# Performance work log

Hardware: AMD Instinct MI355X
Metric: run time of the kernel (lower is better)

The kernel has to match this reference:

```python
import jax, jax.numpy as jnp
import numpy as np

N = 50000      # nodes
E = 800000     # edges
DIM = 64       # dim_h (= input_dim)
H = 4          # heads
D = DIM // H   # per-head dim = 16
EDGE_DIM = 16
L = 5          # conv layers
G = 64         # graphs in batch
FINAL = 1
SCALE = 1.0 / np.sqrt(D)


def setup_inputs() -> dict:
    key = jax.random.key(0)
    ks = jax.random.split(key, 12)
    x = jax.random.normal(ks[0], (N, DIM), jnp.float32)
    edge_index = jax.random.randint(ks[1], (2, E), 0, N, dtype=jnp.int32).astype(jnp.int64)
    edge_attr = jax.random.normal(ks[2], (E, EDGE_DIM), jnp.float32)
    batch = jnp.sort(jax.random.randint(ks[3], (N,), 0, G, dtype=jnp.int32).astype(jnp.int64))
    s = 1.0 / np.sqrt(DIM)
    se = 1.0 / np.sqrt(EDGE_DIM)
    Wq = jax.random.normal(ks[4], (L, DIM, DIM), jnp.float32) * s
    Wk = jax.random.normal(ks[5], (L, DIM, DIM), jnp.float32) * s
    Wv = jax.random.normal(ks[6], (L, DIM, DIM), jnp.float32) * s
    We = jax.random.normal(ks[7], (L, EDGE_DIM, DIM), jnp.float32) * se
    Wskip = jax.random.normal(ks[8], (L, DIM, DIM), jnp.float32) * s
    W1 = jax.random.normal(ks[9], (L * DIM, L * DIM), jnp.float32) * (1.0 / np.sqrt(L * DIM))
    b1 = jnp.zeros((L * DIM,), jnp.float32)
    W2 = jax.random.normal(ks[10], (L * DIM, FINAL), jnp.float32) * (1.0 / np.sqrt(L * DIM))
    b2 = jnp.zeros((FINAL,), jnp.float32)
    return dict(x=x, edge_index=edge_index, edge_attr=edge_attr, batch=batch,
                Wq=Wq, Wk=Wk, Wv=Wv, We=We, Wskip=Wskip, W1=W1, b1=b1, W2=W2, b2=b2)


def _conv(x, Wq, Wk, Wv, We, Wsk, src, dst, edge_attr):
    # Edge-featured multi-head attention conv (EINv1 / TransformerConv-style).
    n = x.shape[0]
    q = (x @ Wq).reshape(n, H, D)[dst]                      # [E,H,D] query from dst node
    e = (edge_attr @ We).reshape(-1, H, D)                  # [E,H,D] edge projection
    k = (x @ Wk).reshape(n, H, D)[src] + e                  # [E,H,D]
    v = (x @ Wv).reshape(n, H, D)[src] + e                  # [E,H,D]
    logits = (q * k).sum(-1) * SCALE                        # [E,H]
    m = jax.ops.segment_max(logits, dst, num_segments=n)    # per-dst-node max
    a = jnp.exp(logits - m[dst])
    s = jax.ops.segment_sum(a, dst, num_segments=n)
    alpha = a / (s[dst] + 1e-16)                            # segment softmax over incoming edges
    agg = jax.ops.segment_sum(alpha[..., None] * v, dst, num_segments=n)  # [N,H,D]
    return agg.reshape(n, H * D) + x @ Wsk                  # root/skip connection


def reference(x, edge_index, edge_attr, batch, Wq, Wk, Wv, We, Wskip, W1, b1, W2, b2):
    src, dst = edge_index[0], edge_index[1]
    counts = jax.ops.segment_sum(jnp.ones((x.shape[0],), x.dtype), batch, num_segments=G)
    denom = jnp.maximum(counts, 1.0)[:, None]
    h = x
    pooled = []
    for l in range(L):  # fixed small layer count
        h = jax.nn.relu(_conv(h, Wq[l], Wk[l], Wv[l], We[l], Wskip[l], src, dst, edge_attr))
        pooled.append(jax.ops.segment_sum(h, batch, num_segments=G) / denom)  # global_mean_pool
    hcat = jnp.concatenate(pooled, axis=1)                  # [G, 5*DIM]
    hid = jax.nn.relu(hcat @ W1 + b1)
    out = hid @ W2 + b2                                     # dropout is identity in eval
    return out.reshape(-1)                                  # flatten -> [G*FINAL]
```

## Files before the change

kernel.cpp:

```cpp
#include <hip/hip_runtime.h>
#include <math.h>

#define NN 50000
#define NE 800000
#define GG 64
#define SCAN_BLK 512
#define SCAN_NB ((NN + SCAN_BLK - 1) / SCAN_BLK)
#define CSR_CAP (NE + 4 * NN)
#define NBLK ((NN + 63) / 64)

typedef unsigned int uint;
typedef unsigned short ushort;
typedef __attribute__((ext_vector_type(8))) short short8v;
typedef __attribute__((ext_vector_type(4))) float f32x4;

__device__ __forceinline__ uint bf16r(float x) {
    uint u = __float_as_uint(x);
    return (u + 0x7fffu + ((u >> 16) & 1u)) >> 16;
}

__device__ __forceinline__ float red8(float x) {
    float t;
    t = __int_as_float(__builtin_amdgcn_update_dpp(0, __float_as_int(x), 0xB1, 0xF, 0xF, 1));
    x += t;
    t = __int_as_float(__builtin_amdgcn_update_dpp(0, __float_as_int(x), 0x4E, 0xF, 0xF, 1));
    x += t;
    t = __int_as_float(__builtin_amdgcn_update_dpp(0, __float_as_int(x), 0x141, 0xF, 0xF, 1));
    x += t;
    return x;
}


__global__ __launch_bounds__(256) void k_degrank(const int* __restrict__ dstv,
                                                 int* __restrict__ deg,
                                                 int* __restrict__ rank) {
    int e = blockIdx.x * 256 + threadIdx.x;
    if (e < NE) rank[e] = atomicAdd(&deg[dstv[e]], 1);
}

__global__ __launch_bounds__(SCAN_BLK) void k_scan1(const int* __restrict__ deg,
                                                    int* __restrict__ locoff,
                                                    int* __restrict__ bsum) {
    __shared__ int sh[SCAN_BLK];
    int tid = threadIdx.x;
    int n = blockIdx.x * SCAN_BLK + tid;
    int v = (n < NN) ? ((deg[n] + 3) & ~3) : 0;
    sh[tid] = v;
    __syncthreads();
    for (int off = 1; off < SCAN_BLK; off <<= 1) {
        int t = (tid >= off) ? sh[tid - off] : 0;
        __syncthreads();
        sh[tid] += t;
        __syncthreads();
    }
    if (n < NN) locoff[n] = sh[tid] - v;
    if (tid == SCAN_BLK - 1) bsum[blockIdx.x] = sh[tid];
}

__global__ void k_scan2b(int* __restrict__ bsum,
                         const int* __restrict__ batch,
                         int* __restrict__ bstart,
                         float* __restrict__ inv,
                         int* __restrict__ ntot) {
    __shared__ int sh[128];
    __shared__ int sb[65];
    int t = threadIdx.x;
    int v = (t < SCAN_NB) ? bsum[t] : 0;
    sh[t] = v;
    __syncthreads();
    for (int off = 1; off < 128; off <<= 1) {
        int u = (t >= off) ? sh[t - off] : 0;
        __syncthreads();
        sh[t] += u;
        __syncthreads();
    }
    if (t < SCAN_NB) bsum[t] = sh[t] - v;
    if (t == 127) ntot[0] = sh[127];
    if (t <= 64) {
        int lo = 0, hi = NN;
        while (lo < hi) { int mid = (lo + hi) >> 1; if (batch[mid] < t) lo = mid + 1; else hi = mid; }
        sb[t] = lo;
        bstart[t] = lo;
    }
    __syncthreads();
    if (t < 64) inv[t] = 1.0f / fmaxf((float)(sb[t + 1] - sb[t]), 1.0f);
}

__global__ __launch_bounds__(256) void k_scatter(const int* __restrict__ srcv,
                                                 const int* __restrict__ dstv,
                                                 const int* __restrict__ locoff,
                                                 const int* __restrict__ bsum,
                                                 const int* __restrict__ rank,
                                                 const int* __restrict__ deg,
                                                 int* __restrict__ srcp,
                                                 int* __restrict__ e2p) {
    int idx = blockIdx.x * 256 + threadIdx.x;
    if (idx < NE) {
        int d = dstv[idx];
        int p = locoff[d] + bsum[d >> 9] + rank[idx];
        srcp[p] = srcv[idx] << 8;
        e2p[p] = idx;
    } else if (idx < NE + NN) {
        int nd = idx - NE;
        int start = locoff[nd] + bsum[nd >> 9];
        int dgn = deg[nd];
        int al = (dgn + 3) & ~3;
        for (int p = start + dgn; p < start + al; ++p) {
            srcp[p] = 0;
            e2p[p] = 0;
        }
    }
}

__global__ __launch_bounds__(256) void k_gather(const int* __restrict__ e2p,
                                                const float* __restrict__ eattr,
                                                uint* __restrict__ aperm32,
                                                const int* __restrict__ ntot) {
    int tot = ntot[0];
    for (int p = blockIdx.x * 256 + threadIdx.x; p < tot; p += gridDim.x * 256) {
        int e = e2p[p];
        const float4* ea = reinterpret_cast<const float4*>(eattr + (size_t)e * 16);
        float4 a = ea[0], b = ea[1], c = ea[2], d4 = ea[3];
        uint u0 = bf16r(a.x) | (bf16r(a.y) << 16);
        uint u1 = bf16r(a.z) | (bf16r(a.w) << 16);
        uint u2 = bf16r(b.x) | (bf16r(b.y) << 16);
        uint u3 = bf16r(b.z) | (bf16r(b.w) << 16);
        uint u4 = bf16r(c.x) | (bf16r(c.y) << 16);
        uint u5 = bf16r(c.z) | (bf16r(c.w) << 16);
        uint u6 = bf16r(d4.x) | (bf16r(d4.y) << 16);
        uint u7 = bf16r(d4.z) | (bf16r(d4.w) << 16);
        uint* base = aperm32 + (size_t)(p >> 2) * 32 + (p & 1) * 16 + ((p >> 1) & 1);
        base[0]  = u0;  base[2]  = u1;  base[4]  = u2;  base[6]  = u3;
        base[8]  = u4;  base[10] = u5;  base[12] = u6;  base[14] = u7;
    }
}


__global__ __launch_bounds__(256) void k_wfrag(const float* __restrict__ Wq,
                                               const float* __restrict__ Wk,
                                               const float* __restrict__ Wv,
                                               const float* __restrict__ Wsk,
                                               const float* __restrict__ We,
                                               ushort* __restrict__ Wf) {
    int t = blockIdx.x * 256 + threadIdx.x;
    if (t >= 5 * 20 * 2 * 64) return;
    int l = t / (20 * 2 * 64);
    int rem = t % (20 * 2 * 64);
    int nt = rem >> 7, s = (rem >> 6) & 1, lane = rem & 63;
    int c = nt * 16 + (lane & 15);
    int k0 = s * 32 + 8 * (lane >> 4);
    int msel = c >> 6, cc = c & 63;
    const float C2 = 0.36067376022224085f;
    ushort o[8];
    if (msel == 4) {
        int hh = cc >> 4, ja = cc & 15;
        const float* we = We + l * 1024 + ja * 64 + hh * 16;
#pragma unroll
        for (int j = 0; j < 8; ++j) {
            const float* wq = Wq + l * 4096 + (k0 + j) * 64 + hh * 16;
            float acc = 0.f;
#pragma unroll
            for (int dd = 0; dd < 16; ++dd) acc += wq[dd] * we[dd];
            o[j] = (ushort)bf16r(acc * C2);
        }
    } else {
        const float* W = (msel == 0) ? Wq + l * 4096 :
                         (msel == 1) ? Wk + l * 4096 :
                         (msel == 2) ? Wv + l * 4096 : Wsk + l * 4096;
        float sc = (msel == 0) ? C2 : 1.0f;
#pragma unroll
        for (int j = 0; j < 8; ++j) o[j] = (ushort)bf16r(W[(k0 + j) * 64 + cc] * sc);
    }
    uint4* dst = reinterpret_cast<uint4*>(Wf + (size_t)t * 8);
    uint4 u;
    u.x = (uint)o[0] | ((uint)o[1] << 16);
    u.y = (uint)o[2] | ((uint)o[3] << 16);
    u.z = (uint)o[4] | ((uint)o[5] << 16);
    u.w = (uint)o[6] | ((uint)o[7] << 16);
    dst[0] = u;
}


template<bool L0>
__global__ __launch_bounds__(256) void k_projm(const float* __restrict__ x,
                                               const ushort* __restrict__ Hin,
                                               const ushort* __restrict__ Wfl,
                                               uint* __restrict__ QQp,
                                               uint* __restrict__ KVp,
                                               ushort* __restrict__ Sbh) {
    int tid = threadIdx.x, lane = tid & 63, wv = tid >> 6;
    int n0 = blockIdx.x * 64;
    int arow = lane & 15, agrp = lane >> 4;

    short8v A[4][2];
#pragma unroll
    for (int mt = 0; mt < 4; ++mt) {
        int node = n0 + mt * 16 + arow;
        if (node >= NN) node = NN - 1;
#pragma unroll
        for (int s = 0; s < 2; ++s) {
            int k0 = s * 32 + agrp * 8;
            if (L0) {
                const float* hp = x + (size_t)node * 64 + k0;
                float4 u = *reinterpret_cast<const float4*>(hp);
                float4 v = *reinterpret_cast<const float4*>(hp + 4);
                short8v a;
                a[0] = (short)bf16r(u.x); a[1] = (short)bf16r(u.y);
                a[2] = (short)bf16r(u.z); a[3] = (short)bf16r(u.w);
                a[4] = (short)bf16r(v.x); a[5] = (short)bf16r(v.y);
                a[6] = (short)bf16r(v.z); a[7] = (short)bf16r(v.w);
                A[mt][s] = a;
            } else {
                A[mt][s] = *reinterpret_cast<const short8v*>(Hin + (size_t)node * 64 + k0);
            }
        }
    }

    int ch = wv * 16 + arow;
    int rb = agrp * 4;
    f32x4 qh[4], kh[4];
    const f32x4 z = {0.f, 0.f, 0.f, 0.f};

#pragma unroll
    for (int ni = 0; ni < 5; ++ni) {
        int ntl = wv + 4 * ni;
        f32x4 acc[4] = {z, z, z, z};
#pragma unroll
        for (int s = 0; s < 2; ++s) {
            short8v B = *reinterpret_cast<const short8v*>(
                Wfl + (((size_t)ntl * 2 + s) * 64 + lane) * 8);
#pragma unroll
            for (int mt = 0; mt < 4; ++mt)
                acc[mt] = __builtin_amdgcn_mfma_f32_16x16x32_bf16(A[mt][s], B, acc[mt], 0, 0, 0);
        }
        if (ni == 0) {
#pragma unroll
            for (int mt = 0; mt < 4; ++mt) qh[mt] = acc[mt];
        } else if (ni == 1) {
#pragma unroll
            for (int mt = 0; mt < 4; ++mt) kh[mt] = acc[mt];
        } else if (ni == 2) {
#pragma unroll
            for (int mt = 0; mt < 4; ++mt)
#pragma unroll
                for (int r = 0; r < 4; ++r) {
                    int node = n0 + mt * 16 + rb + r;
                    if (node < NN)
                        KVp[(size_t)node * 64 + ch] = (bf16r(kh[mt][r]) << 16) | bf16r(acc[mt][r]);
                }
        } else if (ni == 3) {
#pragma unroll
            for (int mt = 0; mt < 4; ++mt)
#pragma unroll
                for (int r = 0; r < 4; ++r) {
                    int node = n0 + mt * 16 + rb + r;
                    if (node < NN) Sbh[(size_t)node * 64 + ch] = (ushort)bf16r(acc[mt][r]);
                }
        } else {
#pragma unroll
            for (int mt = 0; mt < 4; ++mt)
#pragma unroll
                for (int r = 0; r < 4; ++r) {
                    int node = n0 + mt * 16 + rb + r;
                    if (node < NN)
                        QQp[(size_t)node * 64 + ch] = (bf16r(qh[mt][r]) << 16) | bf16r(acc[mt][r]);
                }
        }
    }
}


__global__ __launch_bounds__(256) void k_attn(const uint* __restrict__ QQp,
                                              const uint* __restrict__ KVp,
                                              const ushort* __restrict__ Sbh,
                                              const float* __restrict__ Wel,
                                              const uint* __restrict__ aperm32,
                                              const int* __restrict__ srcp,
                                              const int* __restrict__ locoff,
                                              const int* __restrict__ bsum,
                                              const int* __restrict__ cnt,
                                              ushort* __restrict__ Hout) {
    __shared__ float we[16 * 64];
    int tid = threadIdx.x;
    for (int i = tid; i < 1024; i += 256) we[i] = Wel[i];
    __syncthreads();

    int lane = tid & 63;
    int n = blockIdx.x * 4 + (tid >> 6);
    if (n >= NN) return;

    int pc = lane & 31;
    int eh = lane >> 5;
    int hd = pc >> 3;

    uint2 qq = *reinterpret_cast<const uint2*>(QQp + n * 64 + 2 * pc);
    float qf0  = __uint_as_float(qq.x & 0xffff0000u);
    float qwf0 = __uint_as_float(qq.x << 16);
    float qf1  = __uint_as_float(qq.y & 0xffff0000u);
    float qwf1 = __uint_as_float(qq.y << 16);

    int dg = cnt[n];
    int pos0 = locoff[n] + bsum[n >> 9];
    int npass = (dg + 1) >> 1;
    int nsb = (npass + 1) >> 1;

    const char* kvb = (const char*)KVp + pc * 8;
    const uint2* apb2 = reinterpret_cast<const uint2*>(aperm32 + (size_t)pos0 * 8)
                        + (pc & 7) + eh * 8;

    float s = 0.f, av0 = 0.f, av1 = 0.f, aa0 = 0.f, aa1 = 0.f;

    auto ldidx = [&](int j, int4& s4) {
        s4 = (j < nsb) ? *reinterpret_cast<const int4*>(srcp + pos0 + j * 4)
                       : make_int4(0, 0, 0, 0);
    };
    auto issueSB = [&](int j, const int4& s4, uint2 (&kv)[2], uint2& au) {
        int sn0 = eh ? s4.y : s4.x;
        int sn1 = eh ? s4.w : s4.z;
        kv[0] = *reinterpret_cast<const uint2*>(kvb + sn0);
        kv[1] = *reinterpret_cast<const uint2*>(kvb + sn1);
        au = apb2[(size_t)j * 16];
    };
    auto computeSB = [&](int j, const uint2 (&kv)[2], const uint2& au) {
#pragma unroll
        for (int p = 0; p < 2; ++p) {
            uint a_u = p ? au.y : au.x;
            float kf0 = __uint_as_float(kv[p].x & 0xffff0000u);
            float vf0 = __uint_as_float(kv[p].x << 16);
            float kf1 = __uint_as_float(kv[p].y & 0xffff0000u);
            float vf1 = __uint_as_float(kv[p].y << 16);
            float af0 = __uint_as_float(a_u << 16);
            float af1 = __uint_as_float(a_u & 0xffff0000u);
            float d = qf0 * kf0;
            d = fmaf(qf1, kf1, d);
            d = fmaf(qwf0, af0, d);
            d = fmaf(qwf1, af1, d);
            d = red8(d);
            int ei = j * 4 + p * 2 + eh;
            float l = (ei < dg) ? d : -1e30f;
            float a = __builtin_amdgcn_exp2f(l);
            s += a;
            av0 = fmaf(a, vf0, av0);
            av1 = fmaf(a, vf1, av1);
            aa0 = fmaf(a, af0, aa0);
            aa1 = fmaf(a, af1, aa1);
        }
    };

    int4 s4a, s4b;
    uint2 kvA[2], kvB[2];
    uint2 auA, auB;

    ldidx(0, s4a);
    issueSB(0, s4a, kvA, auA);
    ldidx(1, s4b);

    int sb = 0;
    while (sb + 1 < nsb) {
        issueSB(sb + 1, s4b, kvB, auB);
        ldidx(sb + 2, s4a);
        computeSB(sb, kvA, auA);
        if (sb + 2 < nsb) {
            issueSB(sb + 2, s4a, kvA, auA);
            ldidx(sb + 3, s4b);
        }
        computeSB(sb + 1, kvB, auB);
        sb += 2;
    }
    if (sb < nsb) computeSB(sb, kvA, auA);

    s   += __shfl_xor(s, 32);
    av0 += __shfl_xor(av0, 32);
    av1 += __shfl_xor(av1, 32);
    aa0 += __shfl_xor(aa0, 32);
    aa1 += __shfl_xor(aa1, 32);

    float rden = 1.0f / (s + 1e-16f);
    float e0 = 0.f, e1 = 0.f;
#pragma unroll
    for (int t = 0; t < 8; ++t) {
        float ae = __shfl(aa0, hd * 8 + t, 32);
        float ao = __shfl(aa1, hd * 8 + t, 32);
        float2 wE = *reinterpret_cast<const float2*>(&we[(2 * t) * 64 + 2 * pc]);
        float2 wO = *reinterpret_cast<const float2*>(&we[(2 * t + 1) * 64 + 2 * pc]);
        e0 = fmaf(ae, wE.x, fmaf(ao, wO.x, e0));
        e1 = fmaf(ae, wE.y, fmaf(ao, wO.y, e1));
    }
    uint sbu = *reinterpret_cast<const uint*>(Sbh + (size_t)n * 64 + 2 * pc);
    float sk0 = __uint_as_float(sbu << 16);
    float sk1 = __uint_as_float(sbu & 0xffff0000u);
    float hn0 = fmaxf(fmaf(av0 + e0, rden, sk0), 0.f);
    float hn1 = fmaxf(fmaf(av1 + e1, rden, sk1), 0.f);
    if (lane < 32) {
        uint hw = bf16r(hn0) | (bf16r(hn1) << 16);
        reinterpret_cast<uint*>(Hout)[(size_t)n * 32 + pc] = hw;
    }
}


__global__ __launch_bounds__(512) void k_pool5(const ushort* __restrict__ Hb,
                                               const int* __restrict__ bstart,
                                               const float* __restrict__ inv,
                                               float* __restrict__ hcat) {
    __shared__ float red[512];
    int l = blockIdx.x >> 6, g = blockIdx.x & 63;
    int lo = bstart[g], hi = bstart[g + 1];
    const ushort* H = Hb + (size_t)l * NN * 64;
    int ch = threadIdx.x & 63, ro = threadIdx.x >> 6;
    float acc = 0.f;
    for (int r = lo + ro; r < hi; r += 8)
        acc += __uint_as_float((uint)H[(size_t)r * 64 + ch] << 16);
    red[threadIdx.x] = acc;
    __syncthreads();
    if (ro < 4) red[threadIdx.x] += red[threadIdx.x + 256];
    __syncthreads();
    if (ro < 2) red[threadIdx.x] += red[threadIdx.x + 128];
    __syncthreads();
    if (ro == 0)
        hcat[g * 320 + l * 64 + ch] = (red[ch] + red[64 + ch]) * inv[g];
}


__global__ __launch_bounds__(256) void k_mlp(const float* __restrict__ hcat,
                                             const float* __restrict__ W1,
                                             const float* __restrict__ b1,
                                             const float* __restrict__ W2,
                                             const float* __restrict__ b2,
                                             float* __restrict__ out) {
    __shared__ float hc[320];
    __shared__ float red[256];
    int g = blockIdx.x, tid = threadIdx.x;
    for (int i = tid; i < 320; i += 256) hc[i] = hcat[g * 320 + i];
    __syncthreads();
    float part = 0.f;
    for (int j = tid; j < 320; j += 256) {
        float t = b1[j];
        for (int k = 0; k < 320; ++k) t = fmaf(hc[k], W1[k * 320 + j], t);
        part = fmaf(fmaxf(t, 0.f), W2[j], part);
    }
    red[tid] = part;
    __syncthreads();
    for (int off = 128; off > 0; off >>= 1) {
        if (tid < off) red[tid] += red[tid + off];
        __syncthreads();
    }
    if (tid == 0) out[g] = red[0] + b2[0];
}


extern "C" void kernel_launch(void* const* d_in, const int* in_sizes, int n_in,
                              void* d_out, int out_size, void* d_ws, size_t ws_size,
                              hipStream_t stream) {
    const float* x     = (const float*)d_in[0];
    const int*   ei    = (const int*)d_in[1];
    const float* eattr = (const float*)d_in[2];
    const int*   batch = (const int*)d_in[3];
    const float* Wq    = (const float*)d_in[4];
    const float* Wk    = (const float*)d_in[5];
    const float* Wv    = (const float*)d_in[6];
    const float* We    = (const float*)d_in[7];
    const float* Wsk   = (const float*)d_in[8];
    const float* W1    = (const float*)d_in[9];
    const float* b1    = (const float*)d_in[10];
    const float* W2    = (const float*)d_in[11];
    const float* b2    = (const float*)d_in[12];
    float* out = (float*)d_out;

    const int* srcv = ei;
    const int* dstv = ei + NE;

    float* ws = (float*)d_ws;
    size_t o = 0;
    uint*   QQp = (uint*)(ws + o); o += (size_t)NN * 64;
    uint*   KVp = (uint*)(ws + o); o += (size_t)NN * 64;
    ushort* Sbh = (ushort*)(ws + o); o += (size_t)NN * 32;
    ushort* Hb  = (ushort*)(ws + o); o += (size_t)5 * NN * 64 / 2;
    ushort* Wf  = (ushort*)(ws + o); o += 5 * 20 * 2 * 64 * 8 / 2;
    float*  inv = ws + o;          o += GG;
    float*  hcat = ws + o;         o += GG * 320;
    int*    bstart = (int*)(ws + o); o += 68;
    int*    ntot   = (int*)(ws + o); o += 4;
    int*    deg  = (int*)(ws + o); o += NN;
    int*    srcp = (int*)(ws + o); o += CSR_CAP;
    int*    e2p  = (int*)(ws + o); o += CSR_CAP;
    int*    rank   = (int*)(ws + o); o += NE;
    int*    locoff = (int*)(ws + o); o += NN;
    int*    bsum   = (int*)(ws + o); o += 128;
    ushort* aperm  = (ushort*)(ws + o); o += (size_t)CSR_CAP * 8;

    hipMemsetAsync(deg, 0, (size_t)NN * 4, stream);

    k_degrank<<<(NE + 255) / 256, 256, 0, stream>>>(dstv, deg, rank);
    k_scan1<<<SCAN_NB, SCAN_BLK, 0, stream>>>(deg, locoff, bsum);
    k_scan2b<<<1, 128, 0, stream>>>(bsum, batch, bstart, inv, ntot);
    k_scatter<<<(NE + NN + 255) / 256, 256, 0, stream>>>(srcv, dstv, locoff, bsum,
                                                         rank, deg, srcp, e2p);
    k_gather<<<4096, 256, 0, stream>>>(e2p, eattr, (uint*)aperm, ntot);
    k_wfrag<<<50, 256, 0, stream>>>(Wq, Wk, Wv, Wsk, We, Wf);

    for (int l = 0; l < 5; ++l) {
        const ushort* Wfl = Wf + (size_t)l * 20 * 2 * 64 * 8;
        if (l == 0)
            k_projm<true><<<NBLK, 256, 0, stream>>>(x, Hb, Wfl, QQp, KVp, Sbh);
        else
            k_projm<false><<<NBLK, 256, 0, stream>>>(x, Hb + (size_t)(l - 1) * NN * 64,
                                                     Wfl, QQp, KVp, Sbh);
        k_attn<<<(NN + 3) / 4, 256, 0, stream>>>(QQp, KVp, Sbh,
                                                 We + l * 1024,
                                                 (const uint*)aperm,
                                                 srcp, locoff, bsum, deg,
                                                 Hb + (size_t)l * NN * 64);
    }
    k_pool5<<<320, 512, 0, stream>>>(Hb, bstart, inv, hcat);
    k_mlp<<<GG, 256, 0, stream>>>(hcat, W1, b1, W2, b2, out);
}
```

Baseline: 470.0 us.

## Process four edges per wavefront pass with 16 lanes per edge in attention kernel

The per-node attention kernel now splits the 64-lane wavefront into four 16-lane groups, each handling one edge and four channels per lane, instead of two 32-lane groups handling two channels per lane. K/V gathers become 16-byte loads, the dot-product reduction drops to a 4-lane DPP reduce, and the edge-attribute permutation kernel writes a contiguous 32-byte layout with vector stores. This is meant to cut per-edge instruction count and widen memory accesses. The cost is more registers, an extra cross-lane shuffle stage at the end, and a changed aperm layout that the other kernels must agree with.

```diff
diff --git a/kernel.cpp b/kernel.cpp
--- a/kernel.cpp
+++ b/kernel.cpp
@@ -18,14 +18,14 @@
     uint u = __float_as_uint(x);
     return (u + 0x7fffu + ((u >> 16) & 1u)) >> 16;
 }
-
-__device__ __forceinline__ float red8(float x) {
+__device__ __forceinline__ float bfhi(uint u) { return __uint_as_float(u & 0xffff0000u); }
+__device__ __forceinline__ float bflo(uint u) { return __uint_as_float(u << 16); }
+
+__device__ __forceinline__ float red4(float x) {
     float t;
     t = __int_as_float(__builtin_amdgcn_update_dpp(0, __float_as_int(x), 0xB1, 0xF, 0xF, 1));
     x += t;
     t = __int_as_float(__builtin_amdgcn_update_dpp(0, __float_as_int(x), 0x4E, 0xF, 0xF, 1));
-    x += t;
-    t = __int_as_float(__builtin_amdgcn_update_dpp(0, __float_as_int(x), 0x141, 0xF, 0xF, 1));
     x += t;
     return x;
 }
@@ -121,17 +121,18 @@
         int e = e2p[p];
         const float4* ea = reinterpret_cast<const float4*>(eattr + (size_t)e * 16);
         float4 a = ea[0], b = ea[1], c = ea[2], d4 = ea[3];
-        uint u0 = bf16r(a.x) | (bf16r(a.y) << 16);
-        uint u1 = bf16r(a.z) | (bf16r(a.w) << 16);
-        uint u2 = bf16r(b.x) | (bf16r(b.y) << 16);
-        uint u3 = bf16r(b.z) | (bf16r(b.w) << 16);
-        uint u4 = bf16r(c.x) | (bf16r(c.y) << 16);
-        uint u5 = bf16r(c.z) | (bf16r(c.w) << 16);
-        uint u6 = bf16r(d4.x) | (bf16r(d4.y) << 16);
-        uint u7 = bf16r(d4.z) | (bf16r(d4.w) << 16);
-        uint* base = aperm32 + (size_t)(p >> 2) * 32 + (p & 1) * 16 + ((p >> 1) & 1);
-        base[0]  = u0;  base[2]  = u1;  base[4]  = u2;  base[6]  = u3;
-        base[8]  = u4;  base[10] = u5;  base[12] = u6;  base[14] = u7;
+        uint4 w0, w1;
+        w0.x = bf16r(a.x) | (bf16r(a.y) << 16);
+        w0.y = bf16r(a.z) | (bf16r(a.w) << 16);
+        w0.z = bf16r(b.x) | (bf16r(b.y) << 16);
+        w0.w = bf16r(b.z) | (bf16r(b.w) << 16);
+        w1.x = bf16r(c.x) | (bf16r(c.y) << 16);
+        w1.y = bf16r(c.z) | (bf16r(c.w) << 16);
+        w1.z = bf16r(d4.x) | (bf16r(d4.y) << 16);
+        w1.w = bf16r(d4.z) | (bf16r(d4.w) << 16);
+        uint4* dst = reinterpret_cast<uint4*>(aperm32 + (size_t)p * 8);
+        dst[0] = w0;
+        dst[1] = w1;
     }
 }
 
@@ -289,66 +290,72 @@
     int n = blockIdx.x * 4 + (tid >> 6);
     if (n >= NN) return;
 
-    int pc = lane & 31;
-    int eh = lane >> 5;
-    int hd = pc >> 3;
-
-    uint2 qq = *reinterpret_cast<const uint2*>(QQp + n * 64 + 2 * pc);
-    float qf0  = __uint_as_float(qq.x & 0xffff0000u);
-    float qwf0 = __uint_as_float(qq.x << 16);
-    float qf1  = __uint_as_float(qq.y & 0xffff0000u);
-    float qwf1 = __uint_as_float(qq.y << 16);
+    int lq = lane & 15;
+    int eq = lane >> 4;
+    int hd = lq >> 2;
+
+    uint4 qq = *reinterpret_cast<const uint4*>(QQp + n * 64 + 4 * lq);
+    float qf0 = bfhi(qq.x), qwf0 = bflo(qq.x);
+    float qf1 = bfhi(qq.y), qwf1 = bflo(qq.y);
+    float qf2 = bfhi(qq.z), qwf2 = bflo(qq.z);
+    float qf3 = bfhi(qq.w), qwf3 = bflo(qq.w);
 
     int dg = cnt[n];
     int pos0 = locoff[n] + bsum[n >> 9];
-    int npass = (dg + 1) >> 1;
-    int nsb = (npass + 1) >> 1;
-
-    const char* kvb = (const char*)KVp + pc * 8;
-    const uint2* apb2 = reinterpret_cast<const uint2*>(aperm32 + (size_t)pos0 * 8)
-                        + (pc & 7) + eh * 8;
-
-    float s = 0.f, av0 = 0.f, av1 = 0.f, aa0 = 0.f, aa1 = 0.f;
+    int nsb = (dg + 3) >> 2;
+
+    const char* kvb = (const char*)KVp + lq * 16;
+    const uint2* ap2 = reinterpret_cast<const uint2*>(aperm32)
+                       + (size_t)pos0 * 4 + eq * 4 + (lq & 3);
+
+    float s = 0.f;
+    float av0 = 0.f, av1 = 0.f, av2 = 0.f, av3 = 0.f;
+    float aa0 = 0.f, aa1 = 0.f, aa2 = 0.f, aa3 = 0.f;
 
     auto ldidx = [&](int j, int4& s4) {
         s4 = (j < nsb) ? *reinterpret_cast<const int4*>(srcp + pos0 + j * 4)
                        : make_int4(0, 0, 0, 0);
     };
-    auto issueSB = [&](int j, const int4& s4, uint2 (&kv)[2], uint2& au) {
-        int sn0 = eh ? s4.y : s4.x;
-        int sn1 = eh ? s4.w : s4.z;
-        kv[0] = *reinterpret_cast<const uint2*>(kvb + sn0);
-        kv[1] = *reinterpret_cast<const uint2*>(kvb + sn1);
-        au = apb2[(size_t)j * 16];
+    auto issueSB = [&](int j, const int4& s4, uint4& kv, uint2& au) {
+        int sn = s4.x;
+        if (eq == 1) sn = s4.y;
+        if (eq == 2) sn = s4.z;
+        if (eq == 3) sn = s4.w;
+        kv = *reinterpret_cast<const uint4*>(kvb + sn);
+        au = ap2[(size_t)j * 16];
     };
-    auto computeSB = [&](int j, const uint2 (&kv)[2], const uint2& au) {
-#pragma unroll
-        for (int p = 0; p < 2; ++p) {
-            uint a_u = p ? au.y : au.x;
-            float kf0 = __uint_as_float(kv[p].x & 0xffff0000u);
-            float vf0 = __uint_as_float(kv[p].x << 16);
-            float kf1 = __uint_as_float(kv[p].y & 0xffff0000u);
-            float vf1 = __uint_as_float(kv[p].y << 16);
-            float af0 = __uint_as_float(a_u << 16);
-            float af1 = __uint_as_float(a_u & 0xffff0000u);
-            float d = qf0 * kf0;
-            d = fmaf(qf1, kf1, d);
-            d = fmaf(qwf0, af0, d);
-            d = fmaf(qwf1, af1, d);
-            d = red8(d);
-            int ei = j * 4 + p * 2 + eh;
-            float l = (ei < dg) ? d : -1e30f;
-            float a = __builtin_amdgcn_exp2f(l);
-            s += a;
-            av0 = fmaf(a, vf0, av0);
-            av1 = fmaf(a, vf1, av1);
-            aa0 = fmaf(a, af0, aa0);
-            aa1 = fmaf(a, af1, aa1);
-        }
+    auto computeSB = [&](int j, const uint4& kv, const uint2& au) {
+        float k0 = bfhi(kv.x), v0 = bflo(kv.x);
+        float k1 = bfhi(kv.y), v1 = bflo(kv.y);
+        float k2 = bfhi(kv.z), v2 = bflo(kv.z);
+        float k3 = bfhi(kv.w), v3 = bflo(kv.w);
+        float a0 = bflo(au.x), a1 = bfhi(au.x);
+        float a2 = bflo(au.y), a3 = bfhi(au.y);
+        float d = qf0 * k0;
+        d = fmaf(qf1, k1, d);
+        d = fmaf(qf2, k2, d);
+        d = fmaf(qf3, k3, d);
+        d = fmaf(qwf0, a0, d);
+        d = fmaf(qwf1, a1, d);
+        d = fmaf(qwf2, a2, d);
+        d = fmaf(qwf3, a3, d);
+        d = red4(d);
+        int ei = j * 4 + eq;
+        float l = (ei < dg) ? d : -1e30f;
+        float a = __builtin_amdgcn_exp2f(l);
+        s += a;
+        av0 = fmaf(a, v0, av0);
+        av1 = fmaf(a, v1, av1);
+        av2 = fmaf(a, v2, av2);
+        av3 = fmaf(a, v3, av3);
+        aa0 = fmaf(a, a0, aa0);
+        aa1 = fmaf(a, a1, aa1);
+        aa2 = fmaf(a, a2, aa2);
+        aa3 = fmaf(a, a3, aa3);
     };
 
     int4 s4a, s4b;
-    uint2 kvA[2], kvB[2];
+    uint4 kvA, kvB;
     uint2 auA, auB;
 
     ldidx(0, s4a);
@@ -369,31 +376,45 @@
     }
     if (sb < nsb) computeSB(sb, kvA, auA);
 
-    s   += __shfl_xor(s, 32);
-    av0 += __shfl_xor(av0, 32);
-    av1 += __shfl_xor(av1, 32);
-    aa0 += __shfl_xor(aa0, 32);
-    aa1 += __shfl_xor(aa1, 32);
+    s   += __shfl_xor(s, 16);   s   += __shfl_xor(s, 32);
+    av0 += __shfl_xor(av0, 16); av0 += __shfl_xor(av0, 32);
+    av1 += __shfl_xor(av1, 16); av1 += __shfl_xor(av1, 32);
+    av2 += __shfl_xor(av2, 16); av2 += __shfl_xor(av2, 32);
+    av3 += __shfl_xor(av3, 16); av3 += __shfl_xor(av3, 32);
+    aa0 += __shfl_xor(aa0, 16); aa0 += __shfl_xor(aa0, 32);
+    aa1 += __shfl_xor(aa1, 16); aa1 += __shfl_xor(aa1, 32);
+    aa2 += __shfl_xor(aa2, 16); aa2 += __shfl_xor(aa2, 32);
+    aa3 += __shfl_xor(aa3, 16); aa3 += __shfl_xor(aa3, 32);
 
     float rden = 1.0f / (s + 1e-16f);
-    float e0 = 0.f, e1 = 0.f;
-#pragma unroll
-    for (int t = 0; t < 8; ++t) {
-        float ae = __shfl(aa0, hd * 8 + t, 32);
-        float ao = __shfl(aa1, hd * 8 + t, 32);
-        float2 wE = *reinterpret_cast<const float2*>(&we[(2 * t) * 64 + 2 * pc]);
-        float2 wO = *reinterpret_cast<const float2*>(&we[(2 * t + 1) * 64 + 2 * pc]);
-        e0 = fmaf(ae, wE.x, fmaf(ao, wO.x, e0));
-        e1 = fmaf(ae, wE.y, fmaf(ao, wO.y, e1));
-    }
-    uint sbu = *reinterpret_cast<const uint*>(Sbh + (size_t)n * 64 + 2 * pc);
-    float sk0 = __uint_as_float(sbu << 16);
-    float sk1 = __uint_as_float(sbu & 0xffff0000u);
-    float hn0 = fmaxf(fmaf(av0 + e0, rden, sk0), 0.f);
-    float hn1 = fmaxf(fmaf(av1 + e1, rden, sk1), 0.f);
-    if (lane < 32) {
-        uint hw = bf16r(hn0) | (bf16r(hn1) << 16);
-        reinterpret_cast<uint*>(Hout)[(size_t)n * 32 + pc] = hw;
+    float e0 = 0.f, e1 = 0.f, e2 = 0.f, e3 = 0.f;
+#pragma unroll
+    for (int m = 0; m < 4; ++m) {
+        int sl = hd * 4 + m;
+        float b0 = __shfl(aa0, sl, 16);
+        float b1 = __shfl(aa1, sl, 16);
+        float b2 = __shfl(aa2, sl, 16);
+        float b3 = __shfl(aa3, sl, 16);
+#pragma unroll
+        for (int r = 0; r < 4; ++r) {
+            float bj = (r == 0) ? b0 : (r == 1) ? b1 : (r == 2) ? b2 : b3;
+            float4 w = *reinterpret_cast<const float4*>(&we[(4 * m + r) * 64 + 4 * lq]);
+            e0 = fmaf(bj, w.x, e0);
+            e1 = fmaf(bj, w.y, e1);
+            e2 = fmaf(bj, w.z, e2);
+            e3 = fmaf(bj, w.w, e3);
+        }
+    }
+    uint2 sbu = *reinterpret_cast<const uint2*>(Sbh + (size_t)n * 64 + 4 * lq);
+    float h0 = fmaxf(fmaf(av0 + e0, rden, bflo(sbu.x)), 0.f);
+    float h1 = fmaxf(fmaf(av1 + e1, rden, bfhi(sbu.x)), 0.f);
+    float h2 = fmaxf(fmaf(av2 + e2, rden, bflo(sbu.y)), 0.f);
+    float h3 = fmaxf(fmaf(av3 + e3, rden, bfhi(sbu.y)), 0.f);
+    if (lane < 16) {
+        uint2 hw;
+        hw.x = bf16r(h0) | (bf16r(h1) << 16);
+        hw.y = bf16r(h2) | (bf16r(h3) << 16);
+        reinterpret_cast<uint2*>(Hout)[(size_t)n * 16 + lq] = hw;
     }
 }
 
```

After: 578.9 us. 1.23x slower.
